# Kernel optimization log

Hardware: AMD Instinct MI355X
Metric: run time of the kernel (lower is better)

Reference implementation:

```python
import jax, jax.numpy as jnp
import numpy as np

B, T, D, H = 16, 16384, 128, 256  # batch, seq, embed_dim, hidden_size (num_heads=1)
EPS = 1e-5


def setup_inputs() -> dict:
    key = jax.random.key(0)
    ks = jax.random.split(key, 17)
    w = lambda k, o, i: (jax.random.normal(k, (o, i), jnp.float32) * (1.0 / np.sqrt(i)))
    return {
        "x": jax.random.normal(ks[0], (B, T, D), jnp.float32),
        "Wq": w(ks[1], D, D), "Wk": w(ks[2], D, D), "Wv": w(ks[3], D, D),
        "fmq_w1": w(ks[4], D, D), "fmq_b1": jnp.zeros((D,), jnp.float32),
        "fmq_w2": w(ks[5], D, D), "fmq_b2": jnp.zeros((D,), jnp.float32),
        "fmk_w1": w(ks[6], D, D), "fmk_b1": jnp.zeros((D,), jnp.float32),
        "fmk_w2": w(ks[7], D, D), "fmk_b2": jnp.zeros((D,), jnp.float32),
        "rms_w": jnp.ones((D,), jnp.float32),
        "Wo": w(ks[8], D, D),
        "Wp": w(ks[9], H, D), "bp": jnp.zeros((H,), jnp.float32),
    }


def reference(x, Wq, Wk, Wv, fmq_w1, fmq_b1, fmq_w2, fmq_b2,
              fmk_w1, fmk_b1, fmk_w2, fmk_b2, rms_w, Wo, Wp, bp):
    # q/k/v projections (bias-free, num_heads=1 so head dim == D)
    q = x @ Wq.T
    k = x @ Wk.T
    v = x @ Wv.T
    # Hadamard ('elementwise_product') feature maps
    q = (q @ fmq_w1.T + fmq_b1) * (q @ fmq_w2.T + fmq_b2)
    k = (k @ fmk_w1.T + fmk_b1) * (k @ fmk_w2.T + fmk_b2)
    # non-causal, unnormalized linear attention: o = phi(q) @ (phi(k)^T v)
    S = jnp.einsum('btd,bte->bde', k, v)        # [B, D, D] global KV state
    o = jnp.einsum('btd,bde->bte', q, S)        # [B, T, D]
    # RMSNorm over head_v dim with affine weight
    o = o * jax.lax.rsqrt(jnp.mean(o * o, axis=-1, keepdims=True) + EPS) * rms_w
    # output projection, max-pool over seq, final linear
    o = o @ Wo.T                                 # [B, T, D]
    pooled = jnp.max(o, axis=1)                  # [B, D]
    return pooled @ Wp.T + bp                    # [B, H]
```

## Files before the change

kernel.cpp:

```cpp
#include <hip/hip_runtime.h>
#include <math.h>

#define NB   16
#define TSEQ 16384
#define DD   128
#define HH   256
constexpr float EPS = 1e-5f;

typedef _Float16 h8v __attribute__((ext_vector_type(8)));
typedef _Float16 h4v __attribute__((ext_vector_type(4)));
typedef float    f4v __attribute__((ext_vector_type(4)));

#define MFMA16(a, b, c) __builtin_amdgcn_mfma_f32_16x16x32_f16(a, b, c, 0, 0, 0)

constexpr int SX_S = 136;
constexpr int SW_S = 136;
constexpr int ST_S = 72;

__device__ __forceinline__ void atomicMaxFloat(float* addr, float val) {
    if (val >= 0.0f) atomicMax((int*)addr, __float_as_int(val));
    else             atomicMin((unsigned int*)addr, __float_as_uint(val));
}

__global__ __launch_bounds__(256) void k0_prep(
    const float* __restrict__ Wq, const float* __restrict__ Wk,
    const float* __restrict__ Wv, const float* __restrict__ fq1,
    const float* __restrict__ fq2, const float* __restrict__ fk1,
    const float* __restrict__ fk2, const float* __restrict__ Wo,
    const float* __restrict__ rmsw,
    _Float16* __restrict__ Wh, float* __restrict__ pooled)
{
    const int i = blockIdx.x * 256 + threadIdx.x;
    if (i < 8 * DD * DD) {
        const int mat = i >> 14;
        const int e   = i & (DD * DD - 1);
        const float* srcs[8] = {Wq, Wk, Wv, fq1, fq2, fk1, fk2, Wo};
        float v = srcs[mat][e];
        if (mat == 7) v *= rmsw[e & (DD - 1)];
        Wh[i] = (_Float16)v;
    }
    if (i < NB * DD)      pooled[i] = -INFINITY;
}

constexpr int K1_TM = 128;

__global__ __launch_bounds__(512, 4) void k1_qkvfm(
    const float* __restrict__ x, const _Float16* __restrict__ Wh,
    const float* __restrict__ bq1, const float* __restrict__ bq2,
    const float* __restrict__ bk1, const float* __restrict__ bk2,
    _Float16* __restrict__ qf, _Float16* __restrict__ kfT,
    _Float16* __restrict__ vT)
{
    __shared__ _Float16 sX[K1_TM * SX_S];
    __shared__ _Float16 sCT[K1_TM * SX_S];

    const int tid = threadIdx.x;
    const int wv = tid >> 6;
    const int ln = tid & 63, lm = ln & 15, lq = ln >> 4;
    const long t0 = (long)blockIdx.x * K1_TM;
    const int b = (int)(t0 >> 14), tin = (int)(t0 & (TSEQ - 1));

    const float vb1q = bq1[wv * 16 + lm], vb2q = bq2[wv * 16 + lm];
    const float vb1k = bk1[wv * 16 + lm], vb2k = bk2[wv * 16 + lm];

    {
        const int r = tid >> 2, c0 = (tid & 3) * 32;
        const float* src = x + (t0 + r) * DD + c0;
        _Float16* dst = sX + r * SX_S + c0;
#pragma unroll
        for (int i = 0; i < 8; ++i) {
            const float4 v = *(const float4*)(src + i * 4);
            h4v h; h[0] = (_Float16)v.x; h[1] = (_Float16)v.y;
                   h[2] = (_Float16)v.z; h[3] = (_Float16)v.w;
            *(h4v*)(dst + i * 4) = h;
        }
    }

    auto loadW = [&](int mat, h8v* w) {
        const _Float16* p = Wh + mat * DD * DD + (wv * 16 + lm) * DD + lq * 8;
#pragma unroll
        for (int k0 = 0; k0 < 4; ++k0) w[k0] = *(const h8v*)(p + k0 * 32);
    };
    auto gemm = [&](const _Float16* sA, const h8v* w, f4v* acc) {
#pragma unroll
        for (int k0 = 0; k0 < 4; ++k0)
#pragma unroll
            for (int mt = 0; mt < 8; ++mt) {
                const h8v a = *(const h8v*)(sA + (mt * 16 + lm) * SX_S + k0 * 32 + lq * 8);
                acc[mt] = MFMA16(a, w[k0], acc[mt]);
            }
    };
    auto zero8 = [&](f4v* a) {
#pragma unroll
        for (int i = 0; i < 8; ++i) { a[i][0] = 0.f; a[i][1] = 0.f; a[i][2] = 0.f; a[i][3] = 0.f; }
    };
    auto cToC = [&](const f4v* a) {
#pragma unroll
        for (int mt = 0; mt < 8; ++mt)
#pragma unroll
            for (int r = 0; r < 4; ++r)
                sCT[(mt * 16 + lq * 4 + r) * SX_S + wv * 16 + lm] = (_Float16)a[mt][r];
    };
    auto cToT = [&](const f4v* a) {
#pragma unroll
        for (int mt = 0; mt < 8; ++mt) {
            h4v h;
#pragma unroll
            for (int r = 0; r < 4; ++r) h[r] = (_Float16)a[mt][r];
            *(h4v*)(sCT + (wv * 16 + lm) * SX_S + mt * 16 + lq * 4) = h;
        }
    };
    auto copyC = [&](_Float16* dst0) {
        const int r = tid >> 2, c0 = (tid & 3) * 32;
        const _Float16* s = sCT + r * SX_S + c0;
        _Float16* d = dst0 + (t0 + r) * DD + c0;
        *(h8v*)(d)      = *(const h8v*)(s);
        *(h8v*)(d + 8)  = *(const h8v*)(s + 8);
        *(h8v*)(d + 16) = *(const h8v*)(s + 16);
        *(h8v*)(d + 24) = *(const h8v*)(s + 24);
    };
    auto copyT = [&](_Float16* dst0) {
        const int dd = tid >> 2, c0 = (tid & 3) * 32;
        const _Float16* s = sCT + dd * SX_S + c0;
        _Float16* d = dst0 + ((long)b * DD + dd) * TSEQ + tin + c0;
        *(h8v*)(d)      = *(const h8v*)(s);
        *(h8v*)(d + 8)  = *(const h8v*)(s + 8);
        *(h8v*)(d + 16) = *(const h8v*)(s + 16);
        *(h8v*)(d + 24) = *(const h8v*)(s + 24);
    };

    h8v w[4], w2[4];
    f4v a1[8], a2[8];

    loadW(0, w);
    __syncthreads();

    loadW(3, w2);
    zero8(a1); gemm(sX, w, a1);
    cToC(a1);
    __syncthreads();
    loadW(4, w);
    zero8(a1); gemm(sCT, w2, a1);
    loadW(1, w2);
    zero8(a2); gemm(sCT, w, a2);
    __syncthreads();
#pragma unroll
    for (int mt = 0; mt < 8; ++mt)
#pragma unroll
        for (int r = 0; r < 4; ++r)
            a1[mt][r] = (a1[mt][r] + vb1q) * (a2[mt][r] + vb2q);
    cToC(a1);
    __syncthreads();
    copyC(qf);
    loadW(5, w);
    zero8(a1); gemm(sX, w2, a1);
    __syncthreads();
    cToC(a1);
    __syncthreads();
    loadW(6, w2);
    zero8(a1); gemm(sCT, w, a1);
    loadW(2, w);
    zero8(a2); gemm(sCT, w2, a2);
    __syncthreads();
#pragma unroll
    for (int mt = 0; mt < 8; ++mt)
#pragma unroll
        for (int r = 0; r < 4; ++r)
            a1[mt][r] = (a1[mt][r] + vb1k) * (a2[mt][r] + vb2k);
    cToT(a1);
    __syncthreads();
    copyT(kfT);
    zero8(a1); gemm(sX, w, a1);
    __syncthreads();
    cToT(a1);
    __syncthreads();
    copyT(vT);
}

constexpr int K2_KT = 512;
constexpr int K2_TC = 64;
constexpr int K2_SPLIT = TSEQ / K2_KT;

__global__ __launch_bounds__(256, 4) void k2_kv(const _Float16* __restrict__ kfT,
                                                const _Float16* __restrict__ vT,
                                                float* __restrict__ STf)
{
    __shared__ _Float16 sV[DD * ST_S];
    __shared__ _Float16 sK[DD * ST_S];
    const int tid = threadIdx.x;
    const int wv = tid >> 6, ln = tid & 63, lm = ln & 15, lq = ln >> 4;
    const int b = blockIdx.y;
    const int tbase = blockIdx.x * K2_KT;
    const _Float16* kb = kfT + (long)b * DD * TSEQ;
    const _Float16* vb = vT  + (long)b * DD * TSEQ;
    f4v acc[2][8];
#pragma unroll
    for (int i = 0; i < 2; ++i)
#pragma unroll
        for (int j = 0; j < 8; ++j) { acc[i][j][0]=0.f; acc[i][j][1]=0.f; acc[i][j][2]=0.f; acc[i][j][3]=0.f; }

    for (int tc = 0; tc < K2_KT; tc += K2_TC) {
        const int r = tid >> 1, c0 = (tid & 1) * 32;
        const long g = (long)r * TSEQ + tbase + tc + c0;
#pragma unroll
        for (int i = 0; i < 4; ++i) {
            *(h8v*)(sV + r * ST_S + c0 + i * 8) = *(const h8v*)(vb + g + i * 8);
            *(h8v*)(sK + r * ST_S + c0 + i * 8) = *(const h8v*)(kb + g + i * 8);
        }
        __syncthreads();
#pragma unroll
        for (int k0 = 0; k0 < 2; ++k0) {
            const h8v a0 = *(const h8v*)(sV + ((wv * 2 + 0) * 16 + lm) * ST_S + k0 * 32 + lq * 8);
            const h8v a1 = *(const h8v*)(sV + ((wv * 2 + 1) * 16 + lm) * ST_S + k0 * 32 + lq * 8);
#pragma unroll
            for (int nt = 0; nt < 8; ++nt) {
                const h8v bb = *(const h8v*)(sK + (nt * 16 + lm) * ST_S + k0 * 32 + lq * 8);
                acc[0][nt] = MFMA16(a0, bb, acc[0][nt]);
                acc[1][nt] = MFMA16(a1, bb, acc[1][nt]);
            }
        }
        __syncthreads();
    }
    float* Pb = STf + (long)(b * K2_SPLIT + blockIdx.x) * (DD * DD);
#pragma unroll
    for (int i = 0; i < 2; ++i)
#pragma unroll
        for (int nt = 0; nt < 8; ++nt)
#pragma unroll
            for (int r = 0; r < 4; ++r)
                Pb[((wv * 2 + i) * 16 + lq * 4 + r) * DD + nt * 16 + lm] = acc[i][nt][r];
}

__global__ __launch_bounds__(256) void k2r_reduce(const float* __restrict__ STf,
                                                  _Float16* __restrict__ STh)
{
    const int idx = blockIdx.x * 256 + threadIdx.x;
    const int b = idx >> 14, e = idx & (DD * DD - 1);
    const float* p = STf + (long)b * K2_SPLIT * (DD * DD) + e;
    float s0 = 0.f, s1 = 0.f, s2 = 0.f, s3 = 0.f;
#pragma unroll
    for (int j = 0; j < K2_SPLIT; j += 4) {
        s0 += p[(long)(j + 0) * (DD * DD)];
        s1 += p[(long)(j + 1) * (DD * DD)];
        s2 += p[(long)(j + 2) * (DD * DD)];
        s3 += p[(long)(j + 3) * (DD * DD)];
    }
    STh[idx] = (_Float16)((s0 + s1) + (s2 + s3));
}

constexpr int K3_TC = 128;

__global__ __launch_bounds__(512, 4) void k3_ostage(const _Float16* __restrict__ qf,
                                                    const _Float16* __restrict__ STh,
                                                    const _Float16* __restrict__ WoH,
                                                    float* __restrict__ pooled)
{
    __shared__ _Float16 sA[DD * SW_S];
    __shared__ _Float16 sB[K3_TC * SX_S];
    __shared__ float sPart[2][DD];
    __shared__ float sRed[8][DD];
    const int tid = threadIdx.x;
    const int wv = tid >> 6, ln = tid & 63, lm = ln & 15, lq = ln >> 4;
    const int eg = wv & 1;
    const int tg = wv >> 1;
    const long t0 = (long)blockIdx.x * K3_TC;
    const int b = (int)(t0 >> 14);

    h8v wo[4];
    {
        const int r = tid >> 2, c0 = (tid & 3) * 32;
        const _Float16* src = WoH + r * DD + c0;
        wo[0] = *(const h8v*)(src);
        wo[1] = *(const h8v*)(src + 8);
        wo[2] = *(const h8v*)(src + 16);
        wo[3] = *(const h8v*)(src + 24);
    }
    {
        const int r = tid >> 2, c0 = (tid & 3) * 32;
        const _Float16* src = STh + (long)b * DD * DD + r * DD + c0;
        _Float16* dst = sA + r * SW_S + c0;
        *(h8v*)(dst)      = *(const h8v*)(src);
        *(h8v*)(dst + 8)  = *(const h8v*)(src + 8);
        *(h8v*)(dst + 16) = *(const h8v*)(src + 16);
        *(h8v*)(dst + 24) = *(const h8v*)(src + 24);
    }
    {
        const int r = tid >> 2, c0 = (tid & 3) * 32;
        const _Float16* src = qf + (t0 + r) * DD + c0;
        _Float16* dst = sB + r * SX_S + c0;
        *(h8v*)(dst)      = *(const h8v*)(src);
        *(h8v*)(dst + 8)  = *(const h8v*)(src + 8);
        *(h8v*)(dst + 16) = *(const h8v*)(src + 16);
        *(h8v*)(dst + 24) = *(const h8v*)(src + 24);
    }
    __syncthreads();

    f4v acc[2][4];
#pragma unroll
    for (int i = 0; i < 2; ++i)
#pragma unroll
        for (int j = 0; j < 4; ++j) { acc[i][j][0]=0.f; acc[i][j][1]=0.f; acc[i][j][2]=0.f; acc[i][j][3]=0.f; }
#pragma unroll
    for (int k0 = 0; k0 < 4; ++k0) {
        const h8v bf0 = *(const h8v*)(sB + ((tg * 2 + 0) * 16 + lm) * SX_S + k0 * 32 + lq * 8);
        const h8v bf1 = *(const h8v*)(sB + ((tg * 2 + 1) * 16 + lm) * SX_S + k0 * 32 + lq * 8);
#pragma unroll
        for (int a = 0; a < 4; ++a) {
            const h8v af = *(const h8v*)(sA + ((eg * 4 + a) * 16 + lm) * SW_S + k0 * 32 + lq * 8);
            acc[0][a] = MFMA16(af, bf0, acc[0][a]);
            acc[1][a] = MFMA16(af, bf1, acc[1][a]);
        }
    }
    float ssp[2] = {0.f, 0.f};
#pragma unroll
    for (int bt = 0; bt < 2; ++bt)
#pragma unroll
        for (int a = 0; a < 4; ++a)
#pragma unroll
            for (int r = 0; r < 4; ++r) ssp[bt] += acc[bt][a][r] * acc[bt][a][r];
#pragma unroll
    for (int bt = 0; bt < 2; ++bt) {
        ssp[bt] += __shfl_xor(ssp[bt], 16, 64);
        ssp[bt] += __shfl_xor(ssp[bt], 32, 64);
    }
    if (lq == 0) {
        sPart[eg][tg * 32 + 0 * 16 + lm] = ssp[0];
        sPart[eg][tg * 32 + 1 * 16 + lm] = ssp[1];
    }
    __syncthreads();
    float sc[2];
#pragma unroll
    for (int bt = 0; bt < 2; ++bt) {
        const int t = tg * 32 + bt * 16 + lm;
        sc[bt] = rsqrtf((sPart[0][t] + sPart[1][t]) * (1.0f / DD) + EPS);
    }
#pragma unroll
    for (int bt = 0; bt < 2; ++bt)
#pragma unroll
        for (int a = 0; a < 4; ++a) {
            h4v h;
#pragma unroll
            for (int r = 0; r < 4; ++r) h[r] = (_Float16)(acc[bt][a][r] * sc[bt]);
            *(h4v*)(sB + ((tg * 2 + bt) * 16 + lm) * SX_S + (eg * 4 + a) * 16 + lq * 4) = h;
        }
    {
        const int r = tid >> 2, c0 = (tid & 3) * 32;
        _Float16* dst = sA + r * SW_S + c0;
        *(h8v*)(dst)      = wo[0];
        *(h8v*)(dst + 8)  = wo[1];
        *(h8v*)(dst + 16) = wo[2];
        *(h8v*)(dst + 24) = wo[3];
    }
    __syncthreads();

#pragma unroll
    for (int i = 0; i < 2; ++i)
#pragma unroll
        for (int j = 0; j < 4; ++j) { acc[i][j][0]=0.f; acc[i][j][1]=0.f; acc[i][j][2]=0.f; acc[i][j][3]=0.f; }
#pragma unroll
    for (int k0 = 0; k0 < 4; ++k0) {
        const h8v bf0 = *(const h8v*)(sB + ((tg * 2 + 0) * 16 + lm) * SX_S + k0 * 32 + lq * 8);
        const h8v bf1 = *(const h8v*)(sB + ((tg * 2 + 1) * 16 + lm) * SX_S + k0 * 32 + lq * 8);
#pragma unroll
        for (int a = 0; a < 4; ++a) {
            const h8v af = *(const h8v*)(sA + ((eg * 4 + a) * 16 + lm) * SW_S + k0 * 32 + lq * 8);
            acc[0][a] = MFMA16(af, bf0, acc[0][a]);
            acc[1][a] = MFMA16(af, bf1, acc[1][a]);
        }
    }
#pragma unroll
    for (int a = 0; a < 4; ++a)
#pragma unroll
        for (int r = 0; r < 4; ++r) {
            float m = fmaxf(acc[0][a][r], acc[1][a][r]);
            m = fmaxf(m, __shfl_xor(m, 1, 64));
            m = fmaxf(m, __shfl_xor(m, 2, 64));
            m = fmaxf(m, __shfl_xor(m, 4, 64));
            m = fmaxf(m, __shfl_xor(m, 8, 64));
            if (lm == 0) sRed[wv][(eg * 4 + a) * 16 + lq * 4 + r] = m;
        }
    __syncthreads();
    if (tid < DD) {
        const int egc = tid >> 6;
        float m = sRed[0 * 2 + egc][tid];
#pragma unroll
        for (int g = 1; g < 4; ++g) m = fmaxf(m, sRed[g * 2 + egc][tid]);
        atomicMaxFloat(&pooled[b * DD + tid], m);
    }
}

__global__ __launch_bounds__(HH) void k4_final(const float* __restrict__ pooled,
                                               const float* __restrict__ Wp,
                                               const float* __restrict__ bp,
                                               float* __restrict__ out)
{
    const int b = blockIdx.x;
    const int h = threadIdx.x;
    __shared__ float sp[DD];
    if (h < DD) sp[h] = pooled[b * DD + h];
    __syncthreads();
    float acc = bp[h];
#pragma unroll 8
    for (int d = 0; d < DD; ++d) acc = fmaf(sp[d], Wp[(long)h * DD + d], acc);
    out[b * HH + h] = acc;
}

extern "C" void kernel_launch(void* const* d_in, const int* in_sizes, int n_in,
                              void* d_out, int out_size, void* d_ws, size_t ws_size,
                              hipStream_t stream)
{
    const float* x      = (const float*)d_in[0];
    const float* Wq     = (const float*)d_in[1];
    const float* Wk     = (const float*)d_in[2];
    const float* Wv     = (const float*)d_in[3];
    const float* fmq_w1 = (const float*)d_in[4];
    const float* fmq_b1 = (const float*)d_in[5];
    const float* fmq_w2 = (const float*)d_in[6];
    const float* fmq_b2 = (const float*)d_in[7];
    const float* fmk_w1 = (const float*)d_in[8];
    const float* fmk_b1 = (const float*)d_in[9];
    const float* fmk_w2 = (const float*)d_in[10];
    const float* fmk_b2 = (const float*)d_in[11];
    const float* rms_w  = (const float*)d_in[12];
    const float* Wo     = (const float*)d_in[13];
    const float* Wp     = (const float*)d_in[14];
    const float* bp     = (const float*)d_in[15];
    float* out = (float*)d_out;

    const long nTD = (long)NB * TSEQ * DD;
    _Float16* qf  = (_Float16*)d_ws;
    _Float16* kfT = qf + nTD;
    _Float16* vT  = kfT + nTD;
    _Float16* Wh  = vT + nTD;
    float* STf    = (float*)(Wh + 8 * DD * DD);
    _Float16* STh = (_Float16*)(STf + (long)NB * K2_SPLIT * DD * DD);
    float* pooled = (float*)(STh + NB * DD * DD);

    k0_prep<<<512, 256, 0, stream>>>(Wq, Wk, Wv, fmq_w1, fmq_w2, fmk_w1, fmk_w2,
                                     Wo, rms_w, Wh, pooled);
    k1_qkvfm<<<(NB * TSEQ) / K1_TM, 512, 0, stream>>>(
        x, Wh, fmq_b1, fmq_b2, fmk_b1, fmk_b2, qf, kfT, vT);
    k2_kv<<<dim3(K2_SPLIT, NB), 256, 0, stream>>>(kfT, vT, STf);
    k2r_reduce<<<(NB * DD * DD) / 256, 256, 0, stream>>>(STf, STh);
    k3_ostage<<<(NB * TSEQ) / K3_TC, 512, 0, stream>>>(qf, STh, Wh + 7 * DD * DD, pooled);
    k4_final<<<NB, HH, 0, stream>>>(pooled, Wp, bp, out);
}
```

Measured before the change: 403.5 us.

## Fold feature-map weights into projections and fuse KV-state accumulation into projection kernel

Precomputes fm_w1·Wq, fm_w2·Wq (and the k equivalents) in a small fold kernel, so the projection kernel runs one GEMM per feature-map branch instead of two chained GEMMs. It also fuses the k^T v state accumulation into the projection kernel, with each block looping over 4 tiles of 128 tokens, so kf and v are never written to or read back from global memory. This drops the separate KV kernel and the transposed kf/v buffers in exchange for fewer blocks and an extra fp16 rounding of the folded weights.

New measurement: 490.2 us. 21.5% more time.

```diff
diff --git a/kernel.cpp b/kernel.cpp
--- a/kernel.cpp
+++ b/kernel.cpp
@@ -15,7 +15,9 @@
 
 constexpr int SX_S = 136;
 constexpr int SW_S = 136;
-constexpr int ST_S = 72;
+constexpr int K1_TM = 128;
+constexpr int K1_G  = 4;
+constexpr int K2_SPLIT = 32;
 
 __device__ __forceinline__ void atomicMaxFloat(float* addr, float val) {
     if (val >= 0.0f) atomicMax((int*)addr, __float_as_int(val));
@@ -23,58 +25,90 @@
 }
 
 __global__ __launch_bounds__(256) void k0_prep(
-    const float* __restrict__ Wq, const float* __restrict__ Wk,
-    const float* __restrict__ Wv, const float* __restrict__ fq1,
-    const float* __restrict__ fq2, const float* __restrict__ fk1,
-    const float* __restrict__ fk2, const float* __restrict__ Wo,
+    const float* __restrict__ Wv, const float* __restrict__ Wo,
     const float* __restrict__ rmsw,
     _Float16* __restrict__ Wh, float* __restrict__ pooled)
 {
     const int i = blockIdx.x * 256 + threadIdx.x;
-    if (i < 8 * DD * DD) {
+    if (i < 2 * DD * DD) {
         const int mat = i >> 14;
         const int e   = i & (DD * DD - 1);
-        const float* srcs[8] = {Wq, Wk, Wv, fq1, fq2, fk1, fk2, Wo};
-        float v = srcs[mat][e];
-        if (mat == 7) v *= rmsw[e & (DD - 1)];
-        Wh[i] = (_Float16)v;
-    }
-    if (i < NB * DD)      pooled[i] = -INFINITY;
-}
-
-constexpr int K1_TM = 128;
-
-__global__ __launch_bounds__(512, 4) void k1_qkvfm(
-    const float* __restrict__ x, const _Float16* __restrict__ Wh,
-    const float* __restrict__ bq1, const float* __restrict__ bq2,
-    const float* __restrict__ bk1, const float* __restrict__ bk2,
-    _Float16* __restrict__ qf, _Float16* __restrict__ kfT,
-    _Float16* __restrict__ vT)
-{
-    __shared__ _Float16 sX[K1_TM * SX_S];
-    __shared__ _Float16 sCT[K1_TM * SX_S];
-
+        float v = (mat == 0) ? Wv[e] : Wo[e] * rmsw[e & (DD - 1)];
+        Wh[(4 + mat) * DD * DD + e] = (_Float16)v;
+    }
+    if (i < NB * DD) pooled[i] = -INFINITY;
+}
+
+__global__ __launch_bounds__(256) void k0_fold(
+    const float* __restrict__ Wq, const float* __restrict__ Wk,
+    const float* __restrict__ fq1, const float* __restrict__ fq2,
+    const float* __restrict__ fk1, const float* __restrict__ fk2,
+    _Float16* __restrict__ Wh)
+{
+    __shared__ _Float16 sW[DD * SX_S];
+    __shared__ _Float16 sF[16 * SX_S];
+    const int mat  = blockIdx.x >> 3;
+    const int rblk = blockIdx.x & 7;
+    const float* fms[4] = {fq1, fq2, fk1, fk2};
+    const float* base = (mat < 2) ? Wq : Wk;
+    const float* fm   = fms[mat];
     const int tid = threadIdx.x;
-    const int wv = tid >> 6;
-    const int ln = tid & 63, lm = ln & 15, lq = ln >> 4;
-    const long t0 = (long)blockIdx.x * K1_TM;
-    const int b = (int)(t0 >> 14), tin = (int)(t0 & (TSEQ - 1));
-
-    const float vb1q = bq1[wv * 16 + lm], vb2q = bq2[wv * 16 + lm];
-    const float vb1k = bk1[wv * 16 + lm], vb2k = bk2[wv * 16 + lm];
-
-    {
-        const int r = tid >> 2, c0 = (tid & 3) * 32;
-        const float* src = x + (t0 + r) * DD + c0;
-        _Float16* dst = sX + r * SX_S + c0;
-#pragma unroll
-        for (int i = 0; i < 8; ++i) {
+    {
+        const int r = tid >> 1, c0 = (tid & 1) * 64;
+        const float* src = base + r * DD + c0;
+        _Float16* dst = sW + r * SX_S + c0;
+#pragma unroll
+        for (int i = 0; i < 16; ++i) {
             const float4 v = *(const float4*)(src + i * 4);
             h4v h; h[0] = (_Float16)v.x; h[1] = (_Float16)v.y;
                    h[2] = (_Float16)v.z; h[3] = (_Float16)v.w;
             *(h4v*)(dst + i * 4) = h;
         }
     }
+    {
+        const int r = tid >> 4, c0 = (tid & 15) * 8;
+        const float* src = fm + (rblk * 16 + r) * DD + c0;
+        _Float16* dst = sF + r * SX_S + c0;
+#pragma unroll
+        for (int i = 0; i < 2; ++i) {
+            const float4 v = *(const float4*)(src + i * 4);
+            h4v h; h[0] = (_Float16)v.x; h[1] = (_Float16)v.y;
+                   h[2] = (_Float16)v.z; h[3] = (_Float16)v.w;
+            *(h4v*)(dst + i * 4) = h;
+        }
+    }
+    __syncthreads();
+    const int o2r = tid >> 4, i0 = (tid & 15) * 8;
+    float acc[8] = {0.f, 0.f, 0.f, 0.f, 0.f, 0.f, 0.f, 0.f};
+    for (int o = 0; o < DD; ++o) {
+        const float f = (float)sF[o2r * SX_S + o];
+        const h8v w8 = *(const h8v*)(sW + o * SX_S + i0);
+#pragma unroll
+        for (int j = 0; j < 8; ++j) acc[j] = fmaf(f, (float)w8[j], acc[j]);
+    }
+    h8v hv;
+#pragma unroll
+    for (int j = 0; j < 8; ++j) hv[j] = (_Float16)acc[j];
+    *(h8v*)(Wh + mat * DD * DD + (rblk * 16 + o2r) * DD + i0) = hv;
+}
+
+__global__ __launch_bounds__(512, 4) void k1_mega(
+    const float* __restrict__ x, const _Float16* __restrict__ Wh,
+    const float* __restrict__ bq1, const float* __restrict__ bq2,
+    const float* __restrict__ bk1, const float* __restrict__ bk2,
+    _Float16* __restrict__ qf, float* __restrict__ STf)
+{
+    __shared__ _Float16 sX[K1_TM * SX_S];
+    __shared__ _Float16 sCT[K1_TM * SX_S];
+
+    const int tid = threadIdx.x;
+    const int wv = tid >> 6;
+    const int ln = tid & 63, lm = ln & 15, lq = ln >> 4;
+    const long tb = (long)blockIdx.x * (K1_TM * K1_G);
+    const int b = (int)(tb >> 14);
+
+    const float vb1q = bq1[wv * 16 + lm], vb2q = bq2[wv * 16 + lm];
+    const float vb1k = bk1[wv * 16 + lm], vb2k = bk2[wv * 16 + lm];
 
     auto loadW = [&](int mat, h8v* w) {
         const _Float16* p = Wh + mat * DD * DD + (wv * 16 + lm) * DD + lq * 8;
@@ -94,141 +128,102 @@
 #pragma unroll
         for (int i = 0; i < 8; ++i) { a[i][0] = 0.f; a[i][1] = 0.f; a[i][2] = 0.f; a[i][3] = 0.f; }
     };
-    auto cToC = [&](const f4v* a) {
+
+    f4v accS[8];
+    zero8(accS);
+
+    h8v w[4];
+    f4v a1[8], a2[8];
+
+#pragma unroll 1
+    for (int g = 0; g < K1_G; ++g) {
+        const long t0 = tb + (long)g * K1_TM;
+
+        {
+            const int r = tid >> 2, c0 = (tid & 3) * 32;
+            const float* src = x + (t0 + r) * DD + c0;
+            _Float16* dst = sX + r * SX_S + c0;
+#pragma unroll
+            for (int i = 0; i < 8; ++i) {
+                const float4 v = *(const float4*)(src + i * 4);
+                h4v h; h[0] = (_Float16)v.x; h[1] = (_Float16)v.y;
+                       h[2] = (_Float16)v.z; h[3] = (_Float16)v.w;
+                *(h4v*)(dst + i * 4) = h;
+            }
+        }
+        __syncthreads();
+
+        loadW(0, w);
+        zero8(a1); gemm(sX, w, a1);
+        loadW(1, w);
+        zero8(a2); gemm(sX, w, a2);
 #pragma unroll
         for (int mt = 0; mt < 8; ++mt)
 #pragma unroll
             for (int r = 0; r < 4; ++r)
-                sCT[(mt * 16 + lq * 4 + r) * SX_S + wv * 16 + lm] = (_Float16)a[mt][r];
-    };
-    auto cToT = [&](const f4v* a) {
-#pragma unroll
-        for (int mt = 0; mt < 8; ++mt) {
-            h4v h;
-#pragma unroll
-            for (int r = 0; r < 4; ++r) h[r] = (_Float16)a[mt][r];
-            *(h4v*)(sCT + (wv * 16 + lm) * SX_S + mt * 16 + lq * 4) = h;
-        }
-    };
-    auto copyC = [&](_Float16* dst0) {
-        const int r = tid >> 2, c0 = (tid & 3) * 32;
-        const _Float16* s = sCT + r * SX_S + c0;
-        _Float16* d = dst0 + (t0 + r) * DD + c0;
-        *(h8v*)(d)      = *(const h8v*)(s);
-        *(h8v*)(d + 8)  = *(const h8v*)(s + 8);
-        *(h8v*)(d + 16) = *(const h8v*)(s + 16);
-        *(h8v*)(d + 24) = *(const h8v*)(s + 24);
-    };
-    auto copyT = [&](_Float16* dst0) {
-        const int dd = tid >> 2, c0 = (tid & 3) * 32;
-        const _Float16* s = sCT + dd * SX_S + c0;
-        _Float16* d = dst0 + ((long)b * DD + dd) * TSEQ + tin + c0;
-        *(h8v*)(d)      = *(const h8v*)(s);
-        *(h8v*)(d + 8)  = *(const h8v*)(s + 8);
-        *(h8v*)(d + 16) = *(const h8v*)(s + 16);
-        *(h8v*)(d + 24) = *(const h8v*)(s + 24);
-    };
-
-    h8v w[4], w2[4];
-    f4v a1[8], a2[8];
-
-    loadW(0, w);
-    __syncthreads();
-
-    loadW(3, w2);
-    zero8(a1); gemm(sX, w, a1);
-    cToC(a1);
-    __syncthreads();
-    loadW(4, w);
-    zero8(a1); gemm(sCT, w2, a1);
-    loadW(1, w2);
-    zero8(a2); gemm(sCT, w, a2);
-    __syncthreads();
-#pragma unroll
-    for (int mt = 0; mt < 8; ++mt)
+                a1[mt][r] = (a1[mt][r] + vb1q) * (a2[mt][r] + vb2q);
+#pragma unroll
+        for (int mt = 0; mt < 8; ++mt)
+#pragma unroll
+            for (int r = 0; r < 4; ++r)
+                sCT[(mt * 16 + lq * 4 + r) * SX_S + wv * 16 + lm] = (_Float16)a1[mt][r];
+        __syncthreads();
+        {
+            const int r = tid >> 2, c0 = (tid & 3) * 32;
+            const _Float16* s = sCT + r * SX_S + c0;
+            _Float16* d = qf + (t0 + r) * DD + c0;
+            *(h8v*)(d)      = *(const h8v*)(s);
+            *(h8v*)(d + 8)  = *(const h8v*)(s + 8);
+            *(h8v*)(d + 16) = *(const h8v*)(s + 16);
+            *(h8v*)(d + 24) = *(const h8v*)(s + 24);
+        }
+
+        loadW(2, w);
+        zero8(a1); gemm(sX, w, a1);
+        loadW(3, w);
+        zero8(a2); gemm(sX, w, a2);
+        h4v kh[8];
+#pragma unroll
+        for (int mt = 0; mt < 8; ++mt)
+#pragma unroll
+            for (int r = 0; r < 4; ++r)
+                kh[mt][r] = (_Float16)((a1[mt][r] + vb1k) * (a2[mt][r] + vb2k));
+
+        loadW(4, w);
+        zero8(a2); gemm(sX, w, a2);
+        h4v vh[8];
+#pragma unroll
+        for (int mt = 0; mt < 8; ++mt)
+#pragma unroll
+            for (int r = 0; r < 4; ++r) vh[mt][r] = (_Float16)a2[mt][r];
+        __syncthreads();
+
+#pragma unroll
+        for (int mt = 0; mt < 8; ++mt)
+            *(h4v*)(sCT + (wv * 16 + lm) * SX_S + mt * 16 + lq * 4) = kh[mt];
+#pragma unroll
+        for (int mt = 0; mt < 8; ++mt)
+            *(h4v*)(sX + (wv * 16 + lm) * SX_S + mt * 16 + lq * 4) = vh[mt];
+        __syncthreads();
+
+#pragma unroll
+        for (int k0 = 0; k0 < 4; ++k0) {
+            const h8v av = *(const h8v*)(sX + (wv * 16 + lm) * SX_S + k0 * 32 + lq * 8);
+#pragma unroll
+            for (int nt = 0; nt < 8; ++nt) {
+                const h8v bk = *(const h8v*)(sCT + (nt * 16 + lm) * SX_S + k0 * 32 + lq * 8);
+                accS[nt] = MFMA16(av, bk, accS[nt]);
+            }
+        }
+        __syncthreads();
+    }
+
+    float* Pb = STf + (long)(b * K2_SPLIT + (blockIdx.x & (K2_SPLIT - 1))) * (DD * DD);
+#pragma unroll
+    for (int nt = 0; nt < 8; ++nt)
 #pragma unroll
         for (int r = 0; r < 4; ++r)
-            a1[mt][r] = (a1[mt][r] + vb1q) * (a2[mt][r] + vb2q);
-    cToC(a1);
-    __syncthreads();
-    copyC(qf);
-    loadW(5, w);
-    zero8(a1); gemm(sX, w2, a1);
-    __syncthreads();
-    cToC(a1);
-    __syncthreads();
-    loadW(6, w2);
-    zero8(a1); gemm(sCT, w, a1);
-    loadW(2, w);
-    zero8(a2); gemm(sCT, w2, a2);
-    __syncthreads();
-#pragma unroll
-    for (int mt = 0; mt < 8; ++mt)
-#pragma unroll
-        for (int r = 0; r < 4; ++r)
-            a1[mt][r] = (a1[mt][r] + vb1k) * (a2[mt][r] + vb2k);
-    cToT(a1);
-    __syncthreads();
-    copyT(kfT);
-    zero8(a1); gemm(sX, w, a1);
-    __syncthreads();
-    cToT(a1);
-    __syncthreads();
-    copyT(vT);
-}
-
-constexpr int K2_KT = 512;
-constexpr int K2_TC = 64;
-constexpr int K2_SPLIT = TSEQ / K2_KT;
-
-__global__ __launch_bounds__(256, 4) void k2_kv(const _Float16* __restrict__ kfT,
-                                                const _Float16* __restrict__ vT,
-                                                float* __restrict__ STf)
-{
-    __shared__ _Float16 sV[DD * ST_S];
-    __shared__ _Float16 sK[DD * ST_S];
-    const int tid = threadIdx.x;
-    const int wv = tid >> 6, ln = tid & 63, lm = ln & 15, lq = ln >> 4;
-    const int b = blockIdx.y;
-    const int tbase = blockIdx.x * K2_KT;
-    const _Float16* kb = kfT + (long)b * DD * TSEQ;
-    const _Float16* vb = vT  + (long)b * DD * TSEQ;
-    f4v acc[2][8];
-#pragma unroll
-    for (int i = 0; i < 2; ++i)
-#pragma unroll
-        for (int j = 0; j < 8; ++j) { acc[i][j][0]=0.f; acc[i][j][1]=0.f; acc[i][j][2]=0.f; acc[i][j][3]=0.f; }
-
-    for (int tc = 0; tc < K2_KT; tc += K2_TC) {
-        const int r = tid >> 1, c0 = (tid & 1) * 32;
-        const long g = (long)r * TSEQ + tbase + tc + c0;
-#pragma unroll
-        for (int i = 0; i < 4; ++i) {
-            *(h8v*)(sV + r * ST_S + c0 + i * 8) = *(const h8v*)(vb + g + i * 8);
-            *(h8v*)(sK + r * ST_S + c0 + i * 8) = *(const h8v*)(kb + g + i * 8);
-        }
-        __syncthreads();
-#pragma unroll
-        for (int k0 = 0; k0 < 2; ++k0) {
-            const h8v a0 = *(const h8v*)(sV + ((wv * 2 + 0) * 16 + lm) * ST_S + k0 * 32 + lq * 8);
-            const h8v a1 = *(const h8v*)(sV + ((wv * 2 + 1) * 16 + lm) * ST_S + k0 * 32 + lq * 8);
-#pragma unroll
-            for (int nt = 0; nt < 8; ++nt) {
-                const h8v bb = *(const h8v*)(sK + (nt * 16 + lm) * ST_S + k0 * 32 + lq * 8);
-                acc[0][nt] = MFMA16(a0, bb, acc[0][nt]);
-                acc[1][nt] = MFMA16(a1, bb, acc[1][nt]);
-            }
-        }
-        __syncthreads();
-    }
-    float* Pb = STf + (long)(b * K2_SPLIT + blockIdx.x) * (DD * DD);
-#pragma unroll
-    for (int i = 0; i < 2; ++i)
-#pragma unroll
-        for (int nt = 0; nt < 8; ++nt)
-#pragma unroll
-            for (int r = 0; r < 4; ++r)
-                Pb[((wv * 2 + i) * 16 + lq * 4 + r) * DD + nt * 16 + lm] = acc[i][nt][r];
+            Pb[(wv * 16 + lq * 4 + r) * DD + nt * 16 + lm] = accS[nt][r];
 }
 
 __global__ __launch_bounds__(256) void k2r_reduce(const float* __restrict__ STf,
@@ -429,19 +424,16 @@
 
     const long nTD = (long)NB * TSEQ * DD;
     _Float16* qf  = (_Float16*)d_ws;
-    _Float16* kfT = qf + nTD;
-    _Float16* vT  = kfT + nTD;
-    _Float16* Wh  = vT + nTD;
-    float* STf    = (float*)(Wh + 8 * DD * DD);
+    _Float16* Wh  = qf + nTD;
+    float* STf    = (float*)(Wh + 6 * DD * DD);
     _Float16* STh = (_Float16*)(STf + (long)NB * K2_SPLIT * DD * DD);
     float* pooled = (float*)(STh + NB * DD * DD);
 
-    k0_prep<<<512, 256, 0, stream>>>(Wq, Wk, Wv, fmq_w1, fmq_w2, fmk_w1, fmk_w2,
-                                     Wo, rms_w, Wh, pooled);
-    k1_qkvfm<<<(NB * TSEQ) / K1_TM, 512, 0, stream>>>(
-        x, Wh, fmq_b1, fmq_b2, fmk_b1, fmk_b2, qf, kfT, vT);
-    k2_kv<<<dim3(K2_SPLIT, NB), 256, 0, stream>>>(kfT, vT, STf);
+    k0_prep<<<(2 * DD * DD) / 256, 256, 0, stream>>>(Wv, Wo, rms_w, Wh, pooled);
+    k0_fold<<<32, 256, 0, stream>>>(Wq, Wk, fmq_w1, fmq_w2, fmk_w1, fmk_w2, Wh);
+    k1_mega<<<(NB * TSEQ) / (K1_TM * K1_G), 512, 0, stream>>>(
+        x, Wh, fmq_b1, fmq_b2, fmk_b1, fmk_b2, qf, STf);
     k2r_reduce<<<(NB * DD * DD) / 256, 256, 0, stream>>>(STf, STh);
-    k3_ostage<<<(NB * TSEQ) / K3_TC, 512, 0, stream>>>(qf, STh, Wh + 7 * DD * DD, pooled);
+    k3_ostage<<<(NB * TSEQ) / K3_TC, 512, 0, stream>>>(qf, STh, Wh + 5 * DD * DD, pooled);
     k4_final<<<NB, HH, 0, stream>>>(pooled, Wp, bp, out);
 }
```
